# Kernel tuning notes

Measured on AMD Instinct MI355X. Metric: run time of the kernel, lower is better.

Reference implementation:

```python
import jax, jax.numpy as jnp
import numpy as np

N, E, D_IN, H, D_HEAD = 50000, 800000, 128, 8, 16
SCALE = float(np.sqrt(D_HEAD))


def setup_inputs() -> dict:
    key = jax.random.key(0)
    ks = jax.random.split(key, 9)
    h = jax.random.normal(ks[0], (N, D_IN), dtype=jnp.float32)
    # Q/K/V projection params (torch Linear: y = x @ W.T + b; store as [D_IN, H*D_HEAD])
    s = 1.0 / np.sqrt(D_IN)
    Wq = jax.random.uniform(ks[1], (D_IN, H * D_HEAD), minval=-s, maxval=s, dtype=jnp.float32)
    Wk = jax.random.uniform(ks[2], (D_IN, H * D_HEAD), minval=-s, maxval=s, dtype=jnp.float32)
    Wv = jax.random.uniform(ks[3], (D_IN, H * D_HEAD), minval=-s, maxval=s, dtype=jnp.float32)
    bq = jax.random.uniform(ks[4], (H * D_HEAD,), minval=-s, maxval=s, dtype=jnp.float32)
    bk = jax.random.uniform(ks[5], (H * D_HEAD,), minval=-s, maxval=s, dtype=jnp.float32)
    bv = jax.random.uniform(ks[6], (H * D_HEAD,), minval=-s, maxval=s, dtype=jnp.float32)
    src = jax.random.randint(ks[7], (E,), 0, N, dtype=jnp.int32)
    dst = jax.random.randint(ks[8], (E,), 0, N, dtype=jnp.int32)
    return {"h": h, "Wq": Wq, "bq": bq, "Wk": Wk, "bk": bk, "Wv": Wv, "bv": bv,
            "src": src, "dst": dst}


def reference(h, Wq, bq, Wk, bk, Wv, bv, src, dst):
    n = h.shape[0]
    Q = (h @ Wq + bq).reshape(n, H, D_HEAD)
    K = (h @ Wk + bk).reshape(n, H, D_HEAD)
    V = (h @ Wv + bv).reshape(n, H, D_HEAD)
    # per-edge dot-product score: (K_src * Q_dst).sum(-1), clamped exp
    score = jnp.sum(K[src] * Q[dst], axis=-1, keepdims=True)  # [E, H, 1]
    score = jnp.exp(jnp.clip(score / SCALE, -5.0, 5.0))
    # segment-sum weighted aggregation to destination nodes
    wV = jax.ops.segment_sum(V[src] * score, dst, num_segments=n)   # [N, H, D_HEAD]
    z = jax.ops.segment_sum(score, dst, num_segments=n)              # [N, H, 1]
    return wV / (z + 1e-6)
```

## Files before the change

kernel.cpp:

```cpp
#include <hip/hip_runtime.h>
#include <hip/hip_bf16.h>

#define N_NODES 50000
#define N_EDGES 800000
#define DIN     128
#define HD      128
#define NHEAD   8
#define DHEAD   16

#define BUCKET  64
#define M_PAD   50176
#define ZERO_BLOCKS  196
#define CVTW_BLOCKS  192
#define PROJ3_BLOCKS 1173
#define ESTRIDE      300288
#define AGG_BLOCKS   12500

typedef __attribute__((ext_vector_type(8))) short short8;
typedef __attribute__((ext_vector_type(4))) float float4v;

static __device__ __forceinline__ unsigned short f2bf_bits(float f) {
    __hip_bfloat16 b = __float2bfloat16(f);
    return *reinterpret_cast<unsigned short*>(&b);
}
static __device__ __forceinline__ float bfb(short b) {
    return __uint_as_float(((unsigned int)(unsigned short)b) << 16);
}
static __device__ __forceinline__ short8 cvt8(const float* p) {
    const float4 f0 = *(const float4*)p;
    const float4 f1 = *(const float4*)(p + 4);
    short8 r;
    r[0] = (short)f2bf_bits(f0.x); r[1] = (short)f2bf_bits(f0.y);
    r[2] = (short)f2bf_bits(f0.z); r[3] = (short)f2bf_bits(f0.w);
    r[4] = (short)f2bf_bits(f1.x); r[5] = (short)f2bf_bits(f1.y);
    r[6] = (short)f2bf_bits(f1.z); r[7] = (short)f2bf_bits(f1.w);
    return r;
}

__global__ __launch_bounds__(256) void zero_cvtw_kernel(
    const float* __restrict__ Wq, const float* __restrict__ Wk,
    const float* __restrict__ Wv,
    int* __restrict__ counts, unsigned short* __restrict__ Wt)
{
    const int bid = blockIdx.x;
    if (bid < ZERO_BLOCKS) {
        counts[bid * 256 + threadIdx.x] = 0;
    } else {
        const int i   = (bid - ZERO_BLOCKS) * 256 + threadIdx.x;
        const int n   = i & 127;
        const int k   = (i >> 7) & 127;
        const int mat = i >> 14;
        const float* W = (mat == 0) ? Wq : (mat == 1) ? Wk : Wv;
        Wt[mat * (DIN * HD) + n * DIN + k] = f2bf_bits(W[k * HD + n]);
    }
}

__global__ __launch_bounds__(256) void proj_sort_kernel(
    const float* __restrict__ h,
    const unsigned short* __restrict__ Wt,
    const float* __restrict__ bq, const float* __restrict__ bk,
    const float* __restrict__ bv,
    const int* __restrict__ src, const int* __restrict__ dst,
    int* __restrict__ counts, int* __restrict__ sorted_src,
    __hip_bfloat16* __restrict__ Qb, __hip_bfloat16* __restrict__ KV)
{
    const int bid = blockIdx.x;
    const int tid = threadIdx.x;

    int ee[3], ed[3], es[3], er[3];
    #pragma unroll
    for (int k = 0; k < 3; ++k) {
        ee[k] = k * ESTRIDE + bid * 256 + tid;
        const bool ok = ee[k] < N_EDGES;
        ed[k] = ok ? dst[ee[k]] : 0;
        es[k] = ok ? src[ee[k]] : 0;
    }
    #pragma unroll
    for (int k = 0; k < 3; ++k)
        er[k] = (ee[k] < N_EDGES) ? atomicAdd(&counts[ed[k]], 1) : 0;

    const int mat  = bid % 3;
    const int tile = bid / 3;

    __shared__ unsigned short wlds[DIN * HD];
    {
        const unsigned short* wg = Wt + mat * (DIN * HD);
        #pragma unroll
        for (int it = 0; it < 8; ++it) {
            const int idx = it * 256 + threadIdx.x;
            const int row = idx >> 4;
            const int ch  = idx & 15;
            const int cu  = ((ch >> 2) * 8 + (row >> 4)) * 64
                          + (ch & 3) * 16 + (row & 15);
            *(short8*)&wlds[cu * 8] = *(const short8*)(wg + idx * 8);
        }
    }
    __syncthreads();

    const int wave = threadIdx.x >> 6;
    const int lane = threadIdx.x & 63;
    const int quad = lane >> 4;
    const int l16  = lane & 15;
    const int rowBase = tile * 128 + wave * 32;

    int r0 = rowBase + l16;       if (r0 >= N_NODES) r0 = N_NODES - 1;
    int r1 = rowBase + 16 + l16;  if (r1 >= N_NODES) r1 = N_NODES - 1;

    short8 afr[2][4];
    #pragma unroll
    for (int kc = 0; kc < 4; ++kc) {
        const int ko = kc * 32 + quad * 8;
        afr[0][kc] = cvt8(h + (size_t)r0 * DIN + ko);
        afr[1][kc] = cvt8(h + (size_t)r1 * DIN + ko);
    }

    const float* bias = (mat == 0) ? bq : (mat == 1) ? bk : bv;

    float4v acc[2][8];
    #pragma unroll
    for (int rt = 0; rt < 2; ++rt)
        #pragma unroll
        for (int ct = 0; ct < 8; ++ct)
            acc[rt][ct] = (float4v){0.f, 0.f, 0.f, 0.f};

    #pragma unroll
    for (int kc = 0; kc < 4; ++kc) {
        #pragma unroll
        for (int ct = 0; ct < 8; ++ct) {
            const int cu = (kc * 8 + ct) * 64 + lane;
            const short8 b = *(const short8*)&wlds[cu * 8];
            acc[0][ct] = __builtin_amdgcn_mfma_f32_16x16x32_bf16(afr[0][kc], b, acc[0][ct], 0, 0, 0);
            acc[1][ct] = __builtin_amdgcn_mfma_f32_16x16x32_bf16(afr[1][kc], b, acc[1][ct], 0, 0, 0);
        }
    }

    #pragma unroll
    for (int k = 0; k < 3; ++k)
        if (ee[k] < N_EDGES && er[k] < BUCKET)
            sorted_src[ed[k] * BUCKET + er[k]] = es[k];

    #pragma unroll
    for (int ct = 0; ct < 8; ++ct) {
        const int col = ct * 16 + l16;
        const float bcol = bias[col];
        #pragma unroll
        for (int rt = 0; rt < 2; ++rt) {
            #pragma unroll
            for (int r = 0; r < 4; ++r) {
                const int row = rowBase + rt * 16 + quad * 4 + r;
                if (row < N_NODES) {
                    const float v = acc[rt][ct][r] + bcol;
                    if (mat == 0)
                        Qb[(size_t)row * HD + col] = __float2bfloat16(v);
                    else
                        KV[(size_t)row * 256 + (mat == 2 ? 128 : 0) + col] =
                            __float2bfloat16(v);
                }
            }
        }
    }
}

__global__ __launch_bounds__(256) void aggregate_kernel(
    const __hip_bfloat16* __restrict__ Qb, const __hip_bfloat16* __restrict__ KV,
    const int* __restrict__ counts,
    const int* __restrict__ sorted_src, float* __restrict__ out)
{
    const int w    = threadIdx.x >> 6;
    const int node = blockIdx.x * 4 + w;
    const int lane = threadIdx.x & 63;
    const int quad = lane >> 4;
    const int l16  = lane & 15;
    const int hB   = lane >> 3;

    const int beg = node * BUCKET;
    const int end = beg + counts[node];

    __shared__ float sc_s[4][2][16][9];
    __shared__ int   s_s[4][2][16];

    const short* qrow = (const short*)Qb + (size_t)node * HD;
    const short8 zero8 = {0, 0, 0, 0, 0, 0, 0, 0};
    short8 bfr[4];
    #pragma unroll
    for (int kc = 0; kc < 4; ++kc) {
        const int head = kc * 2 + (quad >> 1);
        const short8 qv = *(const short8*)(qrow + quad * 8 + kc * 32);
        bfr[kc] = (l16 == head) ? qv : zero8;
    }

    const short* kvb = (const short*)KV;
    float acc0 = 0.f, acc1 = 0.f, zacc = 0.f;

    int buf = 0;
    for (int e0 = beg; e0 < end; e0 += 16, buf ^= 1) {
        const int nb = min(16, end - e0);

        const int eidx = e0 + l16;
        const int s = (eidx < end) ? sorted_src[eidx] : 0;
        if (quad == 0) s_s[w][buf][l16] = s;

        const short* kp = kvb + (size_t)s * 256 + quad * 8;
        float4v acc4 = {0.f, 0.f, 0.f, 0.f};
        #pragma unroll
        for (int kc = 0; kc < 4; ++kc) {
            const short8 a = *(const short8*)(kp + kc * 32);
            acc4 = __builtin_amdgcn_mfma_f32_16x16x32_bf16(a, bfr[kc], acc4, 0, 0, 0);
        }
        if (l16 < 8) {
            #pragma unroll
            for (int r = 0; r < 4; ++r) {
                const float d = acc4[r] * 0.25f;
                sc_s[w][buf][quad * 4 + r][l16] =
                    __expf(fminf(fmaxf(d, -5.f), 5.f));
            }
        }
        __threadfence_block();

        int j = 0;
        for (; j + 3 < nb; j += 4) {
            const int s0 = s_s[w][buf][j],     s1 = s_s[w][buf][j + 1];
            const int s2 = s_s[w][buf][j + 2], s3 = s_s[w][buf][j + 3];
            const float c0 = sc_s[w][buf][j][hB],     c1 = sc_s[w][buf][j + 1][hB];
            const float c2 = sc_s[w][buf][j + 2][hB], c3 = sc_s[w][buf][j + 3][hB];
            const unsigned int v0 = *(const unsigned int*)(kvb + (size_t)s0 * 256 + 128 + 2 * lane);
            const unsigned int v1 = *(const unsigned int*)(kvb + (size_t)s1 * 256 + 128 + 2 * lane);
            const unsigned int v2 = *(const unsigned int*)(kvb + (size_t)s2 * 256 + 128 + 2 * lane);
            const unsigned int v3 = *(const unsigned int*)(kvb + (size_t)s3 * 256 + 128 + 2 * lane);
            acc0 = fmaf(__uint_as_float(v0 << 16), c0, acc0);
            acc1 = fmaf(__uint_as_float(v0 & 0xffff0000u), c0, acc1);
            acc0 = fmaf(__uint_as_float(v1 << 16), c1, acc0);
            acc1 = fmaf(__uint_as_float(v1 & 0xffff0000u), c1, acc1);
            acc0 = fmaf(__uint_as_float(v2 << 16), c2, acc0);
            acc1 = fmaf(__uint_as_float(v2 & 0xffff0000u), c2, acc1);
            acc0 = fmaf(__uint_as_float(v3 << 16), c3, acc0);
            acc1 = fmaf(__uint_as_float(v3 & 0xffff0000u), c3, acc1);
            zacc += (c0 + c1) + (c2 + c3);
        }
        for (; j < nb; ++j) {
            const int s0 = s_s[w][buf][j];
            const float c0 = sc_s[w][buf][j][hB];
            const unsigned int v0 = *(const unsigned int*)(kvb + (size_t)s0 * 256 + 128 + 2 * lane);
            acc0 = fmaf(__uint_as_float(v0 << 16), c0, acc0);
            acc1 = fmaf(__uint_as_float(v0 & 0xffff0000u), c0, acc1);
            zacc += c0;
        }
    }

    const float inv = 1.f / (zacc + 1e-6f);
    float2 o;
    o.x = acc0 * inv;
    o.y = acc1 * inv;
    *(float2*)(out + (size_t)node * HD + 2 * lane) = o;
}

extern "C" void kernel_launch(void* const* d_in, const int* in_sizes, int n_in,
                              void* d_out, int out_size, void* d_ws, size_t ws_size,
                              hipStream_t stream)
{
    const float* h   = (const float*)d_in[0];
    const float* Wq  = (const float*)d_in[1];
    const float* bq  = (const float*)d_in[2];
    const float* Wk  = (const float*)d_in[3];
    const float* bk  = (const float*)d_in[4];
    const float* Wv  = (const float*)d_in[5];
    const float* bv  = (const float*)d_in[6];
    const int*   src = (const int*)d_in[7];
    const int*   dst = (const int*)d_in[8];
    float* out = (float*)d_out;

    __hip_bfloat16* Qb = (__hip_bfloat16*)d_ws;
    __hip_bfloat16* KV = Qb + (size_t)N_NODES * HD;
    unsigned short* Wt = (unsigned short*)(KV + (size_t)N_NODES * 256);
    int* counts     = (int*)(Wt + 3 * DIN * HD);
    int* sorted_src = counts + M_PAD;

    zero_cvtw_kernel<<<ZERO_BLOCKS + CVTW_BLOCKS, 256, 0, stream>>>(
        Wq, Wk, Wv, counts, Wt);

    proj_sort_kernel<<<PROJ3_BLOCKS, 256, 0, stream>>>(
        h, Wt, bq, bk, bv, src, dst, counts, sorted_src, Qb, KV);

    aggregate_kernel<<<AGG_BLOCKS, 256, 0, stream>>>(
        Qb, KV, counts, sorted_src, out);
}
```

Measured before the change: 214.1 us.

## Fuse weight conversion into projection kernel and stage outputs through LDS

Removes the separate zero/convert kernel. Each projection block now reads fp32 weights directly, converts them to bf16 into shared memory, and counts are zeroed with hipMemsetAsync. Projection outputs are staged through a padded shared-memory tile so global writes become 16-byte coalesced row stores instead of scattered 2-byte stores. In exchange, every block redoes the weight conversion with strided global reads and gains an extra barrier plus a larger LDS footprint.

```diff
diff --git a/kernel.cpp b/kernel.cpp
--- a/kernel.cpp
+++ b/kernel.cpp
@@ -10,11 +10,11 @@
 
 #define BUCKET  64
 #define M_PAD   50176
-#define ZERO_BLOCKS  196
-#define CVTW_BLOCKS  192
 #define PROJ3_BLOCKS 1173
 #define ESTRIDE      300288
 #define AGG_BLOCKS   12500
+
+#define EPAD    136
 
 typedef __attribute__((ext_vector_type(8))) short short8;
 typedef __attribute__((ext_vector_type(4))) float float4v;
@@ -37,27 +37,10 @@
     return r;
 }
 
-__global__ __launch_bounds__(256) void zero_cvtw_kernel(
+__global__ __launch_bounds__(256) void proj_sort_kernel(
+    const float* __restrict__ h,
     const float* __restrict__ Wq, const float* __restrict__ Wk,
     const float* __restrict__ Wv,
-    int* __restrict__ counts, unsigned short* __restrict__ Wt)
-{
-    const int bid = blockIdx.x;
-    if (bid < ZERO_BLOCKS) {
-        counts[bid * 256 + threadIdx.x] = 0;
-    } else {
-        const int i   = (bid - ZERO_BLOCKS) * 256 + threadIdx.x;
-        const int n   = i & 127;
-        const int k   = (i >> 7) & 127;
-        const int mat = i >> 14;
-        const float* W = (mat == 0) ? Wq : (mat == 1) ? Wk : Wv;
-        Wt[mat * (DIN * HD) + n * DIN + k] = f2bf_bits(W[k * HD + n]);
-    }
-}
-
-__global__ __launch_bounds__(256) void proj_sort_kernel(
-    const float* __restrict__ h,
-    const unsigned short* __restrict__ Wt,
     const float* __restrict__ bq, const float* __restrict__ bk,
     const float* __restrict__ bv,
     const int* __restrict__ src, const int* __restrict__ dst,
@@ -67,6 +50,8 @@
     const int bid = blockIdx.x;
     const int tid = threadIdx.x;
 
+    __shared__ short smem[128 * EPAD];
+
     int ee[3], ed[3], es[3], er[3];
     #pragma unroll
     for (int k = 0; k < 3; ++k) {
@@ -81,24 +66,25 @@
 
     const int mat  = bid % 3;
     const int tile = bid / 3;
-
-    __shared__ unsigned short wlds[DIN * HD];
-    {
-        const unsigned short* wg = Wt + mat * (DIN * HD);
-        #pragma unroll
-        for (int it = 0; it < 8; ++it) {
-            const int idx = it * 256 + threadIdx.x;
-            const int row = idx >> 4;
-            const int ch  = idx & 15;
-            const int cu  = ((ch >> 2) * 8 + (row >> 4)) * 64
-                          + (ch & 3) * 16 + (row & 15);
-            *(short8*)&wlds[cu * 8] = *(const short8*)(wg + idx * 8);
-        }
+    const float* Wg = (mat == 0) ? Wq : (mat == 1) ? Wk : Wv;
+
+    #pragma unroll
+    for (int it = 0; it < 8; ++it) {
+        const int cu   = it * 256 + tid;
+        const int kcct = cu >> 6;
+        const int rem  = cu & 63;
+        const int n    = (kcct & 7) * 16 + (rem & 15);
+        const int k0   = (kcct >> 3) * 32 + (rem >> 4) * 8;
+        short8 w8;
+        #pragma unroll
+        for (int j = 0; j < 8; ++j)
+            w8[j] = (short)f2bf_bits(Wg[(k0 + j) * HD + n]);
+        *(short8*)&smem[cu * 8] = w8;
     }
     __syncthreads();
 
-    const int wave = threadIdx.x >> 6;
-    const int lane = threadIdx.x & 63;
+    const int wave = tid >> 6;
+    const int lane = tid & 63;
     const int quad = lane >> 4;
     const int l16  = lane & 15;
     const int rowBase = tile * 128 + wave * 32;
@@ -128,7 +114,7 @@
         #pragma unroll
         for (int ct = 0; ct < 8; ++ct) {
             const int cu = (kc * 8 + ct) * 64 + lane;
-            const short8 b = *(const short8*)&wlds[cu * 8];
+            const short8 b = *(const short8*)&smem[cu * 8];
             acc[0][ct] = __builtin_amdgcn_mfma_f32_16x16x32_bf16(afr[0][kc], b, acc[0][ct], 0, 0, 0);
             acc[1][ct] = __builtin_amdgcn_mfma_f32_16x16x32_bf16(afr[1][kc], b, acc[1][ct], 0, 0, 0);
         }
@@ -139,6 +125,7 @@
         if (ee[k] < N_EDGES && er[k] < BUCKET)
             sorted_src[ed[k] * BUCKET + er[k]] = es[k];
 
+    __syncthreads();
     #pragma unroll
     for (int ct = 0; ct < 8; ++ct) {
         const int col = ct * 16 + l16;
@@ -147,16 +134,28 @@
         for (int rt = 0; rt < 2; ++rt) {
             #pragma unroll
             for (int r = 0; r < 4; ++r) {
-                const int row = rowBase + rt * 16 + quad * 4 + r;
-                if (row < N_NODES) {
-                    const float v = acc[rt][ct][r] + bcol;
-                    if (mat == 0)
-                        Qb[(size_t)row * HD + col] = __float2bfloat16(v);
-                    else
-                        KV[(size_t)row * 256 + (mat == 2 ? 128 : 0) + col] =
-                            __float2bfloat16(v);
-                }
+                const int lr = wave * 32 + rt * 16 + quad * 4 + r;
+                smem[lr * EPAD + col] =
+                    (short)f2bf_bits(acc[rt][ct][r] + bcol);
             }
+        }
+    }
+    __syncthreads();
+
+    short* qs = (short*)Qb;
+    short* kvs = (short*)KV;
+    #pragma unroll
+    for (int it = 0; it < 8; ++it) {
+        const int idx = it * 256 + tid;
+        const int lr  = idx >> 4;
+        const int ch  = idx & 15;
+        const int row = tile * 128 + lr;
+        if (row < N_NODES) {
+            const short8 v = *(const short8*)&smem[lr * EPAD + ch * 8];
+            if (mat == 0)
+                *(short8*)(qs + (size_t)row * HD + ch * 8) = v;
+            else
+                *(short8*)(kvs + (size_t)row * 256 + (mat == 2 ? 128 : 0) + ch * 8) = v;
         }
     }
 }
@@ -271,15 +270,13 @@
 
     __hip_bfloat16* Qb = (__hip_bfloat16*)d_ws;
     __hip_bfloat16* KV = Qb + (size_t)N_NODES * HD;
-    unsigned short* Wt = (unsigned short*)(KV + (size_t)N_NODES * 256);
-    int* counts     = (int*)(Wt + 3 * DIN * HD);
+    int* counts     = (int*)(KV + (size_t)N_NODES * 256);
     int* sorted_src = counts + M_PAD;
 
-    zero_cvtw_kernel<<<ZERO_BLOCKS + CVTW_BLOCKS, 256, 0, stream>>>(
-        Wq, Wk, Wv, counts, Wt);
+    hipMemsetAsync(counts, 0, M_PAD * sizeof(int), stream);
 
     proj_sort_kernel<<<PROJ3_BLOCKS, 256, 0, stream>>>(
-        h, Wt, bq, bk, bv, src, dst, counts, sorted_src, Qb, KV);
+        h, Wq, Wk, Wv, bq, bk, bv, src, dst, counts, sorted_src, Qb, KV);
 
     aggregate_kernel<<<AGG_BLOCKS, 256, 0, stream>>>(
         Qb, KV, counts, sorted_src, out);
```

Measured after the change: 203.2 us. 5.1% less time.
